# Optimization experiments

Measured on AMD Instinct MI355X. Metric: run time of the kernel, lower is better.

The kernel has to match this reference:

```python
import jax, jax.numpy as jnp
import numpy as np

N_NODES = 100000
N_EDGES = 1600000


def _spmm(row, col, val, x, n):
    # out[i] = sum_{e: row[e]==i} val[e] * x[col[e]]  (sparse adj @ dense x)
    return jax.ops.segment_sum(val[:, None] * x[col], row, num_segments=n)


def setup_inputs() -> dict:
    key = jax.random.key(0)
    ks = jax.random.split(key, 6)
    x = jax.random.normal(ks[0], (N_NODES, 128), dtype=jnp.float32)
    edge_row = jnp.sort(jax.random.randint(ks[1], (N_EDGES,), 0, N_NODES, dtype=jnp.int64))
    edge_col = jax.random.randint(ks[2], (N_EDGES,), 0, N_NODES, dtype=jnp.int64)
    # glorot-initialized linear layers (pyg Linear with weight_initializer='glorot')
    W0 = jax.random.normal(ks[3], (128, 128), dtype=jnp.float32) * np.sqrt(2.0 / (128 + 128))
    b0 = jnp.zeros((128,), dtype=jnp.float32)
    W1 = jax.random.normal(ks[4], (128, 64), dtype=jnp.float32) * np.sqrt(2.0 / (128 + 64))
    b1 = jnp.zeros((64,), dtype=jnp.float32)
    return {"x": x, "edge_row": edge_row, "edge_col": edge_col,
            "W0": W0, "b0": b0, "W1": W1, "b1": b1}


def reference(x, edge_row, edge_col, W0, b0, W1, b1):
    n = x.shape[0]
    # adj_norm: symmetric GCN normalization D^{-1/2} A D^{-1/2}
    ones = jnp.ones(edge_row.shape[0], dtype=x.dtype)
    deg = jax.ops.segment_sum(ones, edge_row, num_segments=n)
    dinv = jnp.where(deg > 0, jax.lax.rsqrt(jnp.maximum(deg, 1.0)), 0.0).astype(x.dtype)
    val = dinv[edge_row] * dinv[edge_col]
    # layer 0: linear -> SpMM -> relu (dropout is a no-op in inference/eval)
    h = x @ W0 + b0
    h = _spmm(edge_row, edge_col, val, h, n)
    h = jax.nn.relu(h)
    # layer 1: linear -> SpMM
    h = h @ W1 + b1
    h = _spmm(edge_row, edge_col, val, h, n)
    return jax.nn.log_softmax(h, axis=-1)
```

## Files before the change

kernel.cpp:

```cpp
#include <hip/hip_runtime.h>
#include <hip/hip_bf16.h>

#define NN 100000
#define NE 1600000

typedef __bf16 bf16x8 __attribute__((ext_vector_type(8)));
typedef float  f32x4  __attribute__((ext_vector_type(4)));

__global__ __launch_bounds__(256) void build_rowptr(const int* __restrict__ row,
                                                    int* __restrict__ row_ptr,
                                                    int E, int N) {
    int e = blockIdx.x * blockDim.x + threadIdx.x;
    if (e >= E) return;
    int r  = row[e];
    int rp = (e == 0) ? -1 : row[e - 1];
    for (int i = rp + 1; i <= r; ++i) row_ptr[i] = e;
    if (e == E - 1) {
        for (int i = r + 1; i <= N; ++i) row_ptr[i] = E;
    }
}

__global__ __launch_bounds__(256) void compute_dinv(const int* __restrict__ row_ptr,
                                                    float* __restrict__ dinv, int N) {
    int i = blockIdx.x * blockDim.x + threadIdx.x;
    if (i >= N) return;
    int deg = row_ptr[i + 1] - row_ptr[i];
    dinv[i] = (deg > 0) ? rsqrtf((float)deg) : 0.0f;
}

__global__ __launch_bounds__(256) void pack_wt(const float* __restrict__ W,
                                               __hip_bfloat16* __restrict__ Wt,
                                               int K, int N) {
    int idx = blockIdx.x * 256 + threadIdx.x;
    if (idx >= K * N) return;
    int n = idx / K, k = idx - n * K;
    Wt[idx] = __float2bfloat16(W[(size_t)k * N + n]);
}

template <int NO, typename InT>
__global__ __launch_bounds__(256) void gemm_mfma(const InT* __restrict__ X,
                                                 const __hip_bfloat16* __restrict__ Wt,
                                                 const float* __restrict__ bias,
                                                 const float* __restrict__ rowscale,
                                                 __hip_bfloat16* __restrict__ out, int M) {
    constexpr int LDA = 136;
    constexpr int NT  = NO / 16;
    __shared__ short As[64 * LDA];
    __shared__ short Ws[NO * LDA];

    const int t = threadIdx.x;
    const int w = t >> 6, lane = t & 63;
    const int l15 = lane & 15, quad = lane >> 4;
    const int rbase = blockIdx.x * 64;

    for (int i = t; i < NO * 16; i += 256) {
        int n = i >> 4, c8 = (i & 15) << 3;
        *(uint4*)&Ws[n * LDA + c8] = ((const uint4*)Wt)[i];
    }
    if constexpr (sizeof(InT) == 4) {
        for (int i = t; i < 2048; i += 256) {
            int r = i >> 5, c = (i & 31) << 2;
            float4 xv = make_float4(0.f, 0.f, 0.f, 0.f);
            if (rbase + r < M) xv = ((const float4*)X)[(size_t)rbase * 32 + i];
            union { __hip_bfloat162 h; unsigned int u; } p0, p1;
            p0.h = __float22bfloat162_rn(make_float2(xv.x, xv.y));
            p1.h = __float22bfloat162_rn(make_float2(xv.z, xv.w));
            *(uint2*)&As[r * LDA + c] = make_uint2(p0.u, p1.u);
        }
    } else {
        for (int i = t; i < 1024; i += 256) {
            int r = i >> 4, c8 = (i & 15) << 3;
            uint4 v = make_uint4(0u, 0u, 0u, 0u);
            if (rbase + r < M) v = ((const uint4*)X)[(size_t)rbase * 16 + i];
            *(uint4*)&As[r * LDA + c8] = v;
        }
    }
    __syncthreads();

    f32x4 acc[NT];
#pragma unroll
    for (int nt = 0; nt < NT; ++nt) {
        float bv = bias[nt * 16 + l15];
        acc[nt][0] = bv; acc[nt][1] = bv; acc[nt][2] = bv; acc[nt][3] = bv;
    }

    const int arow = w * 16 + l15;
#pragma unroll
    for (int kc = 0; kc < 4; ++kc) {
        bf16x8 af = *(const bf16x8*)&As[arow * LDA + kc * 32 + quad * 8];
#pragma unroll
        for (int nt = 0; nt < NT; ++nt) {
            bf16x8 bfr = *(const bf16x8*)&Ws[(nt * 16 + l15) * LDA + kc * 32 + quad * 8];
            acc[nt] = __builtin_amdgcn_mfma_f32_16x16x32_bf16(af, bfr, acc[nt], 0, 0, 0);
        }
    }

#pragma unroll
    for (int r = 0; r < 4; ++r) {
        int grow = rbase + w * 16 + quad * 4 + r;
        if (grow < M) {
            float sc = rowscale[grow];
#pragma unroll
            for (int nt = 0; nt < NT; ++nt)
                out[(size_t)grow * NO + nt * 16 + l15] = __float2bfloat16(acc[nt][r] * sc);
        }
    }
}

__global__ __launch_bounds__(256) void spmm_relu_128(const int* __restrict__ row_ptr,
                                                     const int* __restrict__ col,
                                                     const float* __restrict__ dinv,
                                                     const unsigned int* __restrict__ H,
                                                     __hip_bfloat16* __restrict__ out, int N) {
    const int lane = threadIdx.x & 63;
    int i = __builtin_amdgcn_readfirstlane(blockIdx.x * 4 + (threadIdx.x >> 6));
    if (i >= N) return;
    const float di = dinv[i];
    const int e0 = __builtin_amdgcn_readfirstlane(row_ptr[i]);
    const int e1 = __builtin_amdgcn_readfirstlane(row_ptr[i + 1]);
    float accx = 0.f, accy = 0.f;
    int e = e0;
    for (; e + 8 <= e1; e += 8) {
#pragma unroll
        for (int j = 0; j < 8; ++j) {
            int c = __builtin_amdgcn_readfirstlane(col[e + j]);
            unsigned int u = H[(size_t)c * 64 + lane];
            accx += __uint_as_float(u << 16);
            accy += __uint_as_float(u & 0xffff0000u);
        }
    }
    for (; e < e1; ++e) {
        int c = __builtin_amdgcn_readfirstlane(col[e]);
        unsigned int u = H[(size_t)c * 64 + lane];
        accx += __uint_as_float(u << 16);
        accy += __uint_as_float(u & 0xffff0000u);
    }
    accx = fmaxf(accx * di, 0.f);
    accy = fmaxf(accy * di, 0.f);
    *(__hip_bfloat162*)&out[(size_t)i * 128 + 2 * lane] =
        __float22bfloat162_rn(make_float2(accx, accy));
}

__global__ __launch_bounds__(256) void spmm_logsoftmax_64(const int* __restrict__ row_ptr,
                                                          const int* __restrict__ col,
                                                          const float* __restrict__ dinv,
                                                          const unsigned short* __restrict__ H,
                                                          float* __restrict__ out, int N) {
    const int lane = threadIdx.x & 63;
    int i = __builtin_amdgcn_readfirstlane(blockIdx.x * 4 + (threadIdx.x >> 6));
    if (i >= N) return;
    const float di = dinv[i];
    const int e0 = __builtin_amdgcn_readfirstlane(row_ptr[i]);
    const int e1 = __builtin_amdgcn_readfirstlane(row_ptr[i + 1]);
    float acc = 0.f;
    int e = e0;
    for (; e + 8 <= e1; e += 8) {
#pragma unroll
        for (int j = 0; j < 8; ++j) {
            int c = __builtin_amdgcn_readfirstlane(col[e + j]);
            acc += __uint_as_float((unsigned int)H[(size_t)c * 64 + lane] << 16);
        }
    }
    for (; e < e1; ++e) {
        int c = __builtin_amdgcn_readfirstlane(col[e]);
        acc += __uint_as_float((unsigned int)H[(size_t)c * 64 + lane] << 16);
    }
    acc *= di;
    float m = acc;
#pragma unroll
    for (int off = 32; off > 0; off >>= 1)
        m = fmaxf(m, __shfl_xor(m, off, 64));
    float ex = __expf(acc - m);
    float s = ex;
#pragma unroll
    for (int off = 32; off > 0; off >>= 1)
        s += __shfl_xor(s, off, 64);
    out[(size_t)i * 64 + lane] = acc - m - __logf(s);
}

extern "C" void kernel_launch(void* const* d_in, const int* in_sizes, int n_in,
                              void* d_out, int out_size, void* d_ws, size_t ws_size,
                              hipStream_t stream) {
    const float* x    = (const float*)d_in[0];
    const int*   erow = (const int*)d_in[1];
    const int*   ecol = (const int*)d_in[2];
    const float* W0   = (const float*)d_in[3];
    const float* b0   = (const float*)d_in[4];
    const float* W1   = (const float*)d_in[5];
    const float* b1   = (const float*)d_in[6];
    float* out = (float*)d_out;

    char* ws = (char*)d_ws;
    int*             row_ptr = (int*)ws;
    float*           dinv    = (float*)(ws + (512u << 10));
    __hip_bfloat16*  h0b     = (__hip_bfloat16*)(ws + (1u << 20));
    __hip_bfloat16*  h1b     = (__hip_bfloat16*)(ws + 27000000u);
    __hip_bfloat16*  h2b     = (__hip_bfloat16*)(ws + 53000000u);
    __hip_bfloat16*  Wt0     = (__hip_bfloat16*)(ws + 66000000u);
    __hip_bfloat16*  Wt1     = (__hip_bfloat16*)(ws + 66100000u);

    build_rowptr<<<(NE + 255) / 256, 256, 0, stream>>>(erow, row_ptr, NE, NN);
    compute_dinv<<<(NN + 255) / 256, 256, 0, stream>>>(row_ptr, dinv, NN);
    pack_wt<<<(128 * 128 + 255) / 256, 256, 0, stream>>>(W0, Wt0, 128, 128);
    pack_wt<<<(128 * 64 + 255) / 256, 256, 0, stream>>>(W1, Wt1, 128, 64);

    gemm_mfma<128, float><<<(NN + 63) / 64, 256, 0, stream>>>(x, Wt0, b0, dinv, h0b, NN);
    spmm_relu_128<<<(NN + 3) / 4, 256, 0, stream>>>(row_ptr, ecol, dinv,
                                                    (const unsigned int*)h0b, h1b, NN);
    gemm_mfma<64, __hip_bfloat16><<<(NN + 63) / 64, 256, 0, stream>>>(h1b, Wt1, b1, dinv, h2b, NN);
    spmm_logsoftmax_64<<<(NN + 3) / 4, 256, 0, stream>>>(row_ptr, ecol, dinv,
                                                         (const unsigned short*)h2b, out, NN);
}
```

Before: 254.1 us.

## Swizzle GEMM LDS, stage outputs for vector stores, batch SpMM gathers, fuse weight packing

Several changes land together. The GEMM now processes 128-row tiles with 512 threads and an XOR-swizzled LDS layout in place of padding. Its output is staged through LDS so each row is written with 16-byte vector stores instead of scattered 2-byte stores. Both SpMM kernels gain a 16-edge unrolled path that issues all gathers before accumulating, to keep more loads in flight. The two weight-packing launches are merged into one. Larger blocks and LDS use may lower occupancy, and the extra registers for batched gathers may do the same.

```diff
diff --git a/kernel.cpp b/kernel.cpp
--- a/kernel.cpp
+++ b/kernel.cpp
@@ -28,51 +28,57 @@
     dinv[i] = (deg > 0) ? rsqrtf((float)deg) : 0.0f;
 }
 
-__global__ __launch_bounds__(256) void pack_wt(const float* __restrict__ W,
-                                               __hip_bfloat16* __restrict__ Wt,
-                                               int K, int N) {
+__global__ __launch_bounds__(256) void pack_weights(const float* __restrict__ W0,
+                                                    const float* __restrict__ W1,
+                                                    __hip_bfloat16* __restrict__ Wt0,
+                                                    __hip_bfloat16* __restrict__ Wt1) {
     int idx = blockIdx.x * 256 + threadIdx.x;
-    if (idx >= K * N) return;
-    int n = idx / K, k = idx - n * K;
-    Wt[idx] = __float2bfloat16(W[(size_t)k * N + n]);
+    if (idx < 128 * 128) {
+        int n = idx >> 7, k = idx & 127;
+        Wt0[idx] = __float2bfloat16(W0[(size_t)k * 128 + n]);
+    } else if (idx < 128 * 128 + 64 * 128) {
+        int r = idx - 128 * 128;
+        int n = r >> 7, k = r & 127;
+        Wt1[r] = __float2bfloat16(W1[(size_t)k * 64 + n]);
+    }
 }
 
 template <int NO, typename InT>
-__global__ __launch_bounds__(256) void gemm_mfma(const InT* __restrict__ X,
+__global__ __launch_bounds__(512) void gemm_mfma(const InT* __restrict__ X,
                                                  const __hip_bfloat16* __restrict__ Wt,
                                                  const float* __restrict__ bias,
                                                  const float* __restrict__ rowscale,
                                                  __hip_bfloat16* __restrict__ out, int M) {
-    constexpr int LDA = 136;
-    constexpr int NT  = NO / 16;
-    __shared__ short As[64 * LDA];
-    __shared__ short Ws[NO * LDA];
+    constexpr int NT = NO / 16;
+    __shared__ unsigned short As[128 * 128];
+    __shared__ unsigned short Ws[NO * 128];
 
     const int t = threadIdx.x;
     const int w = t >> 6, lane = t & 63;
     const int l15 = lane & 15, quad = lane >> 4;
-    const int rbase = blockIdx.x * 64;
-
-    for (int i = t; i < NO * 16; i += 256) {
-        int n = i >> 4, c8 = (i & 15) << 3;
-        *(uint4*)&Ws[n * LDA + c8] = ((const uint4*)Wt)[i];
+    const int rbase = blockIdx.x * 128;
+
+    for (int i = t; i < NO * 16; i += 512) {
+        int n = i >> 4, g = i & 15;
+        *(uint4*)&Ws[n * 128 + ((g ^ (n & 7)) << 3)] = ((const uint4*)Wt)[i];
     }
     if constexpr (sizeof(InT) == 4) {
-        for (int i = t; i < 2048; i += 256) {
-            int r = i >> 5, c = (i & 31) << 2;
+        for (int i = t; i < 4096; i += 512) {
+            int r = i >> 5, c2 = i & 31;
             float4 xv = make_float4(0.f, 0.f, 0.f, 0.f);
             if (rbase + r < M) xv = ((const float4*)X)[(size_t)rbase * 32 + i];
             union { __hip_bfloat162 h; unsigned int u; } p0, p1;
             p0.h = __float22bfloat162_rn(make_float2(xv.x, xv.y));
             p1.h = __float22bfloat162_rn(make_float2(xv.z, xv.w));
-            *(uint2*)&As[r * LDA + c] = make_uint2(p0.u, p1.u);
+            int phys = ((c2 >> 1) ^ (r & 7));
+            *(uint2*)&As[r * 128 + (phys << 3) + ((c2 & 1) << 2)] = make_uint2(p0.u, p1.u);
         }
     } else {
-        for (int i = t; i < 1024; i += 256) {
-            int r = i >> 4, c8 = (i & 15) << 3;
+        for (int i = t; i < 2048; i += 512) {
+            int r = i >> 4, g = i & 15;
             uint4 v = make_uint4(0u, 0u, 0u, 0u);
             if (rbase + r < M) v = ((const uint4*)X)[(size_t)rbase * 16 + i];
-            *(uint4*)&As[r * LDA + c8] = v;
+            *(uint4*)&As[r * 128 + ((g ^ (r & 7)) << 3)] = v;
         }
     }
     __syncthreads();
@@ -85,24 +91,42 @@
     }
 
     const int arow = w * 16 + l15;
+    const int asw  = arow & 7;
 #pragma unroll
     for (int kc = 0; kc < 4; ++kc) {
-        bf16x8 af = *(const bf16x8*)&As[arow * LDA + kc * 32 + quad * 8];
+        bf16x8 af = *(const bf16x8*)&As[arow * 128 + (((kc * 4 + quad) ^ asw) << 3)];
 #pragma unroll
         for (int nt = 0; nt < NT; ++nt) {
-            bf16x8 bfr = *(const bf16x8*)&Ws[(nt * 16 + l15) * LDA + kc * 32 + quad * 8];
+            int brow = nt * 16 + l15;
+            bf16x8 bfr = *(const bf16x8*)&Ws[brow * 128 + (((kc * 4 + quad) ^ (brow & 7)) << 3)];
             acc[nt] = __builtin_amdgcn_mfma_f32_16x16x32_bf16(af, bfr, acc[nt], 0, 0, 0);
         }
     }
 
-#pragma unroll
-    for (int r = 0; r < 4; ++r) {
-        int grow = rbase + w * 16 + quad * 4 + r;
+    __hip_bfloat16* Cs = (__hip_bfloat16*)As;
+#pragma unroll
+    for (int r4 = 0; r4 < 4; ++r4) {
+        int lrow = w * 16 + quad * 4 + r4;
+        int grow = rbase + lrow;
+        float sc = (grow < M) ? rowscale[grow] : 0.f;
+#pragma unroll
+        for (int nt = 0; nt < NT; ++nt) {
+            int ct = nt * 16 + l15;
+            Cs[lrow * 128 + ((((ct >> 3) ^ (lrow & 7)) << 3)) + (ct & 7)] =
+                __float2bfloat16(acc[nt][r4] * sc);
+        }
+    }
+    constexpr int RJ  = NO / 8;
+    constexpr int CNT = (16 * RJ) / 64;
+#pragma unroll
+    for (int k = 0; k < CNT; ++k) {
+        int idx = k * 64 + lane;
+        int lr16 = idx / RJ, j = idx % RJ;
+        int lrow = w * 16 + lr16;
+        int grow = rbase + lrow;
         if (grow < M) {
-            float sc = rowscale[grow];
-#pragma unroll
-            for (int nt = 0; nt < NT; ++nt)
-                out[(size_t)grow * NO + nt * 16 + l15] = __float2bfloat16(acc[nt][r] * sc);
+            uint4 v = *(const uint4*)&Cs[lrow * 128 + ((j ^ (lrow & 7)) << 3)];
+            *(uint4*)&out[(size_t)grow * NO + (j << 3)] = v;
         }
     }
 }
@@ -120,13 +144,30 @@
     const int e1 = __builtin_amdgcn_readfirstlane(row_ptr[i + 1]);
     float accx = 0.f, accy = 0.f;
     int e = e0;
+    for (; e + 16 <= e1; e += 16) {
+        unsigned int u[16];
+#pragma unroll
+        for (int j = 0; j < 16; ++j) {
+            int c = __builtin_amdgcn_readfirstlane(col[e + j]);
+            u[j] = H[(size_t)c * 64 + lane];
+        }
+#pragma unroll
+        for (int j = 0; j < 16; ++j) {
+            accx += __uint_as_float(u[j] << 16);
+            accy += __uint_as_float(u[j] & 0xffff0000u);
+        }
+    }
     for (; e + 8 <= e1; e += 8) {
+        unsigned int u[8];
 #pragma unroll
         for (int j = 0; j < 8; ++j) {
             int c = __builtin_amdgcn_readfirstlane(col[e + j]);
-            unsigned int u = H[(size_t)c * 64 + lane];
-            accx += __uint_as_float(u << 16);
-            accy += __uint_as_float(u & 0xffff0000u);
+            u[j] = H[(size_t)c * 64 + lane];
+        }
+#pragma unroll
+        for (int j = 0; j < 8; ++j) {
+            accx += __uint_as_float(u[j] << 16);
+            accy += __uint_as_float(u[j] & 0xffff0000u);
         }
     }
     for (; e < e1; ++e) {
@@ -154,12 +195,27 @@
     const int e1 = __builtin_amdgcn_readfirstlane(row_ptr[i + 1]);
     float acc = 0.f;
     int e = e0;
+    for (; e + 16 <= e1; e += 16) {
+        unsigned short u[16];
+#pragma unroll
+        for (int j = 0; j < 16; ++j) {
+            int c = __builtin_amdgcn_readfirstlane(col[e + j]);
+            u[j] = H[(size_t)c * 64 + lane];
+        }
+#pragma unroll
+        for (int j = 0; j < 16; ++j)
+            acc += __uint_as_float((unsigned int)u[j] << 16);
+    }
     for (; e + 8 <= e1; e += 8) {
+        unsigned short u[8];
 #pragma unroll
         for (int j = 0; j < 8; ++j) {
             int c = __builtin_amdgcn_readfirstlane(col[e + j]);
-            acc += __uint_as_float((unsigned int)H[(size_t)c * 64 + lane] << 16);
-        }
+            u[j] = H[(size_t)c * 64 + lane];
+        }
+#pragma unroll
+        for (int j = 0; j < 8; ++j)
+            acc += __uint_as_float((unsigned int)u[j] << 16);
     }
     for (; e < e1; ++e) {
         int c = __builtin_amdgcn_readfirstlane(col[e]);
@@ -201,13 +257,12 @@
 
     build_rowptr<<<(NE + 255) / 256, 256, 0, stream>>>(erow, row_ptr, NE, NN);
     compute_dinv<<<(NN + 255) / 256, 256, 0, stream>>>(row_ptr, dinv, NN);
-    pack_wt<<<(128 * 128 + 255) / 256, 256, 0, stream>>>(W0, Wt0, 128, 128);
-    pack_wt<<<(128 * 64 + 255) / 256, 256, 0, stream>>>(W1, Wt1, 128, 64);
-
-    gemm_mfma<128, float><<<(NN + 63) / 64, 256, 0, stream>>>(x, Wt0, b0, dinv, h0b, NN);
+    pack_weights<<<(128 * 128 + 64 * 128 + 255) / 256, 256, 0, stream>>>(W0, W1, Wt0, Wt1);
+
+    gemm_mfma<128, float><<<(NN + 127) / 128, 512, 0, stream>>>(x, Wt0, b0, dinv, h0b, NN);
     spmm_relu_128<<<(NN + 3) / 4, 256, 0, stream>>>(row_ptr, ecol, dinv,
                                                     (const unsigned int*)h0b, h1b, NN);
-    gemm_mfma<64, __hip_bfloat16><<<(NN + 63) / 64, 256, 0, stream>>>(h1b, Wt1, b1, dinv, h2b, NN);
+    gemm_mfma<64, __hip_bfloat16><<<(NN + 127) / 128, 512, 0, stream>>>(h1b, Wt1, b1, dinv, h2b, NN);
     spmm_logsoftmax_64<<<(NN + 3) / 4, 256, 0, stream>>>(row_ptr, ecol, dinv,
                                                          (const unsigned short*)h2b, out, NN);
 }
```

New measurement: 249.1 us. About the same (-2.0%).
